# Performance work log

Hardware: AMD Instinct MI355X
Metric: run time of the kernel (lower is better)

## Reference

```python
import jax, jax.numpy as jnp
import numpy as np

H = 16      # num_heads
D = 64      # internal_emb_dim (head dim)
E = 1024    # q/kv input embedding dim
NEG_INF = float('-inf')


def setup_inputs() -> dict:
    key = jax.random.key(0)
    ks = jax.random.split(key, 10)
    B, S = 2, 2048
    sc_in = 1.0 / np.sqrt(E)            # kaiming-uniform-ish scale
    sc_h = 1.0 / np.sqrt(H * D)
    return {
        'x':    jax.random.normal(ks[0], (B, S, E), jnp.float32),
        'ln_g': jnp.ones((E,), jnp.float32),
        'ln_b': jnp.zeros((E,), jnp.float32),
        # weights stored [in, out] (transpose of torch layout), biases zero-init per module
        'wq': jax.random.uniform(ks[1], (E, H * D), jnp.float32, -sc_in, sc_in),
        'bq': jnp.zeros((H * D,), jnp.float32),
        'wk': jax.random.uniform(ks[2], (E, H * D), jnp.float32, -sc_in, sc_in),
        'bk': jnp.zeros((H * D,), jnp.float32),
        'wv': jax.random.uniform(ks[3], (E, H * D), jnp.float32, -sc_in, sc_in),
        'bv': jnp.zeros((H * D,), jnp.float32),
        'w0': jax.random.uniform(ks[4], (H * D, E), jnp.float32, -sc_h, sc_h),
        'b0': jnp.zeros((E,), jnp.float32),
    }


def _layer_norm(x, g, b, eps=1e-5):
    mu = jnp.mean(x, axis=-1, keepdims=True)
    var = jnp.mean(jnp.square(x - mu), axis=-1, keepdims=True)
    return (x - mu) * jax.lax.rsqrt(var + eps) * g + b


def reference(x, ln_g, ln_b, wq, bq, wk, bk, wv, bv, w0, b0):
    B, S, _ = x.shape
    residual = x
    xn = _layer_norm(x, ln_g, ln_b)
    # projections -> [B, H, S, D]
    q = (xn @ wq + bq).reshape(B, S, H, D).transpose(0, 2, 1, 3)
    k = (xn @ wk + bk).reshape(B, S, H, D).transpose(0, 2, 1, 3)
    v = (xn @ wv + bv).reshape(B, S, H, D).transpose(0, 2, 1, 3)
    scores = jnp.einsum('bhqd,bhkd->bhqk', q, k) / jnp.sqrt(jnp.float32(D))
    # custom mask: strictly lower triangle (j < i) filled with -inf
    mask = jnp.tril(jnp.ones((S, S), bool), k=-1)
    scores = jnp.where(mask, NEG_INF, scores)
    a = jax.nn.softmax(scores, axis=-1)
    h = jnp.einsum('bhqk,bhkd->bhqd', a, v)
    h = h.transpose(0, 2, 1, 3).reshape(B, S, H * D)
    return h @ w0 + b0 + residual
```

## Files before the change

kernel.cpp:

```cpp
#include <hip/hip_runtime.h>
#include <hip/hip_bf16.h>
#include <stdint.h>

#define S_LEN 2048
#define E_DIM 1024
#define NHEAD 16
#define DHEAD 64
#define NB 2
#define NROWS (NB * S_LEN)

typedef __attribute__((ext_vector_type(8))) short bf16x8;
typedef __attribute__((ext_vector_type(4))) float f32x4;

__device__ __forceinline__ unsigned short f2b(float f) {
    union { __hip_bfloat16 h; unsigned short u; } cv;
    cv.h = __float2bfloat16(f);
    return cv.u;
}

__device__ __forceinline__ void gload_lds16(const void* g, void* l) {
    __builtin_amdgcn_global_load_lds(
        (const __attribute__((address_space(1))) unsigned int*)g,
        (__attribute__((address_space(3))) unsigned int*)l, 16, 0, 0);
}

__global__ __launch_bounds__(256) void wtrans_kernel(
    const float* __restrict__ wq, const float* __restrict__ wk,
    const float* __restrict__ wv, const float* __restrict__ w0,
    unsigned short* __restrict__ wqT, unsigned short* __restrict__ wkT,
    unsigned short* __restrict__ wvT, unsigned short* __restrict__ w0T) {
    const int z = blockIdx.z;
    const float* W = (z == 0) ? wq : (z == 1) ? wk : (z == 2) ? wv : w0;
    unsigned short* WT = (z == 0) ? wqT : (z == 1) ? wkT : (z == 2) ? wvT : w0T;
    const int k0 = blockIdx.x * 64;
    const int n0 = blockIdx.y * 64;
    __shared__ float tile[64][69];
    const int t = threadIdx.x;
    const int rowq = t >> 4;
    const int cc4 = (t & 15) * 4;
    #pragma unroll
    for (int rr = 0; rr < 4; ++rr) {
        const int r = rr * 16 + rowq;
        const float4 v = *reinterpret_cast<const float4*>(W + (size_t)(k0 + r) * E_DIM + n0 + cc4);
        tile[r][cc4 + 0] = v.x; tile[r][cc4 + 1] = v.y;
        tile[r][cc4 + 2] = v.z; tile[r][cc4 + 3] = v.w;
    }
    __syncthreads();
    #pragma unroll
    for (int rr = 0; rr < 4; ++rr) {
        const int n = rr * 16 + rowq;
        ushort4 o;
        o.x = f2b(tile[cc4 + 0][n]);
        o.y = f2b(tile[cc4 + 1][n]);
        o.z = f2b(tile[cc4 + 2][n]);
        o.w = f2b(tile[cc4 + 3][n]);
        *reinterpret_cast<ushort4*>(WT + (size_t)(n0 + n) * E_DIM + k0 + cc4) = o;
    }
}

__global__ __launch_bounds__(256) void ln_kernel(const float* __restrict__ x,
    const float* __restrict__ g, const float* __restrict__ bt,
    unsigned short* __restrict__ xn) {
    const int row = blockIdx.x;
    const int t = threadIdx.x;
    const float4 v = reinterpret_cast<const float4*>(x + (size_t)row * E_DIM)[t];
    float s  = v.x + v.y + v.z + v.w;
    float ss = v.x * v.x + v.y * v.y + v.z * v.z + v.w * v.w;
    #pragma unroll
    for (int off = 32; off > 0; off >>= 1) {
        s  += __shfl_down(s, off);
        ss += __shfl_down(ss, off);
    }
    __shared__ float red[8];
    if ((t & 63) == 0) { red[t >> 6] = s; red[(t >> 6) + 4] = ss; }
    __syncthreads();
    s  = red[0] + red[1] + red[2] + red[3];
    ss = red[4] + red[5] + red[6] + red[7];
    const float mu  = s * (1.0f / E_DIM);
    const float var = ss * (1.0f / E_DIM) - mu * mu;
    const float rs  = rsqrtf(var + 1e-5f);
    const float4 gv = reinterpret_cast<const float4*>(g)[t];
    const float4 bv = reinterpret_cast<const float4*>(bt)[t];
    ushort4 o;
    o.x = f2b((v.x - mu) * rs * gv.x + bv.x);
    o.y = f2b((v.y - mu) * rs * gv.y + bv.y);
    o.z = f2b((v.z - mu) * rs * gv.z + bv.z);
    o.w = f2b((v.w - mu) * rs * gv.w + bv.w);
    reinterpret_cast<ushort4*>(xn + (size_t)row * E_DIM)[t] = o;
}

__device__ __forceinline__ void gemm128_mainloop(
    const unsigned short* __restrict__ A, const unsigned short* __restrict__ BT,
    int m0, int n0, unsigned short* As, unsigned short* Bs, f32x4 acc[4][4]) {
    const int t = threadIdx.x;
    const int l = t & 63;
    const int w = t >> 6;
    const int wr = w >> 1, wc = w & 1;
    const int lr = l >> 3;
    const int gs = (l & 7) ^ lr;
    const int il = l & 15;
    const int kq = l >> 4;

    for (int kt = 0; kt < E_DIM; kt += 64) {
        __syncthreads();
        #pragma unroll
        for (int c = 0; c < 4; ++c) {
            const int cc = w * 4 + c;
            gload_lds16(A + (size_t)(m0 + cc * 8 + lr) * E_DIM + kt + gs * 8, As + cc * 512);
        }
        #pragma unroll
        for (int c = 0; c < 4; ++c) {
            const int cc = w * 4 + c;
            gload_lds16(BT + (size_t)(n0 + cc * 8 + lr) * E_DIM + kt + gs * 8, Bs + cc * 512);
        }
        __syncthreads();
        #pragma unroll
        for (int ks = 0; ks < 2; ++ks) {
            bf16x8 af[4], bfr[4];
            #pragma unroll
            for (int mi = 0; mi < 4; ++mi) {
                const int r = wr * 64 + mi * 16 + il;
                af[mi] = *reinterpret_cast<const bf16x8*>(As + r * 64 + ((ks * 4 + kq) ^ (r & 7)) * 8);
            }
            #pragma unroll
            for (int ni = 0; ni < 4; ++ni) {
                const int r = wc * 64 + ni * 16 + il;
                bfr[ni] = *reinterpret_cast<const bf16x8*>(Bs + r * 64 + ((ks * 4 + kq) ^ (r & 7)) * 8);
            }
            #pragma unroll
            for (int mi = 0; mi < 4; ++mi)
                #pragma unroll
                for (int ni = 0; ni < 4; ++ni)
                    acc[mi][ni] = __builtin_amdgcn_mfma_f32_16x16x32_bf16(af[mi], bfr[ni], acc[mi][ni], 0, 0, 0);
        }
    }
}

__global__ __launch_bounds__(256) void qkv_kernel(
    const unsigned short* __restrict__ xn,
    const unsigned short* __restrict__ wqT, const float* __restrict__ bq,
    const unsigned short* __restrict__ wkT, const float* __restrict__ bk,
    const unsigned short* __restrict__ wvT, const float* __restrict__ bv,
    unsigned short* __restrict__ qo, unsigned short* __restrict__ ko,
    unsigned short* __restrict__ vo) {
    __shared__ __align__(16) unsigned short As[8192];
    __shared__ __align__(16) unsigned short Bs[8192];
    const int mat = blockIdx.z;
    const unsigned short* BT = (mat == 0) ? wqT : (mat == 1) ? wkT : wvT;
    const float* bias = (mat == 0) ? bq : (mat == 1) ? bk : bv;
    const int m0 = blockIdx.x * 128, n0 = blockIdx.y * 128;

    const f32x4 ZERO = {0.f, 0.f, 0.f, 0.f};
    f32x4 acc[4][4];
    #pragma unroll
    for (int i = 0; i < 4; ++i)
        #pragma unroll
        for (int j = 0; j < 4; ++j) acc[i][j] = ZERO;

    gemm128_mainloop(xn, BT, m0, n0, As, Bs, acc);

    const int t = threadIdx.x, l = t & 63, w = t >> 6;
    const int wr = w >> 1, wc = w & 1;
    const int il = l & 15, kq = l >> 4;
    const int b = m0 >> 11;
    const float qsc = (mat == 0) ? 0.125f : 1.0f;
    unsigned short* outp = (mat == 0) ? qo : ko;

    #pragma unroll
    for (int ni = 0; ni < 4; ++ni) {
        const int n = n0 + wc * 64 + ni * 16 + il;
        const int h = n >> 6, d = n & 63;
        const float bb = bias[n];
        #pragma unroll
        for (int mi = 0; mi < 4; ++mi) {
            const int mbase = m0 + wr * 64 + mi * 16 + kq * 4;
            const int sbase = mbase & (S_LEN - 1);
            if (mat == 2) {
                ushort4 o;
                o.x = f2b(acc[mi][ni][0] + bb);
                o.y = f2b(acc[mi][ni][1] + bb);
                o.z = f2b(acc[mi][ni][2] + bb);
                o.w = f2b(acc[mi][ni][3] + bb);
                *reinterpret_cast<ushort4*>(vo + ((size_t)(b * NHEAD + h) * DHEAD + d) * S_LEN + sbase) = o;
            } else {
                #pragma unroll
                for (int r = 0; r < 4; ++r)
                    outp[((size_t)(b * NHEAD + h) * S_LEN + sbase + r) * DHEAD + d] =
                        f2b((acc[mi][ni][r] + bb) * qsc);
            }
        }
    }
}

__device__ __forceinline__ void attn_tile128(
    const unsigned short* __restrict__ Kc, const unsigned short* __restrict__ Vc,
    unsigned short* __restrict__ Pw, const bf16x8* qf,
    float* m, float* lsum, f32x4* o,
    int il, int kq, int w, int qi0, int kt0, bool do_mask) {
    const f32x4 ZERO = {0.f, 0.f, 0.f, 0.f};
    f32x4 s[8];
    #pragma unroll
    for (int nf = 0; nf < 8; ++nf) s[nf] = ZERO;
    #pragma unroll
    for (int ks = 0; ks < 2; ++ks)
        #pragma unroll
        for (int nf = 0; nf < 8; ++nf) {
            const int j = nf * 16 + il;
            const bf16x8 kf = *reinterpret_cast<const bf16x8*>(
                Kc + j * 64 + (((ks * 4 + kq) ^ (il & 7)) * 8));
            s[nf] = __builtin_amdgcn_mfma_f32_16x16x32_bf16(qf[ks], kf, s[nf], 0, 0, 0);
        }
    if (do_mask) {
        #pragma unroll
        for (int nf = 0; nf < 8; ++nf) {
            const int j = kt0 + nf * 16 + il;
            #pragma unroll
            for (int r = 0; r < 4; ++r) {
                const int i = qi0 + w * 16 + kq * 4 + r;
                if (j < i) s[nf][r] = -INFINITY;
            }
        }
    }
    float tm[4];
    #pragma unroll
    for (int r = 0; r < 4; ++r) {
        float v = s[0][r];
        #pragma unroll
        for (int nf = 1; nf < 8; ++nf) v = fmaxf(v, s[nf][r]);
        tm[r] = v;
    }
    #pragma unroll
    for (int msk = 8; msk; msk >>= 1)
        #pragma unroll
        for (int r = 0; r < 4; ++r)
            tm[r] = fmaxf(tm[r], __shfl_xor(tm[r], msk));
    float sc_[4];
    #pragma unroll
    for (int r = 0; r < 4; ++r) {
        const float nm = fmaxf(m[r], tm[r]);
        sc_[r] = __expf(m[r] - nm);
        m[r] = nm;
    }
    float ps[4] = {0.f, 0.f, 0.f, 0.f};
    #pragma unroll
    for (int nf = 0; nf < 8; ++nf)
        #pragma unroll
        for (int r = 0; r < 4; ++r) {
            const float pv = __expf(s[nf][r] - m[r]);
            ps[r] += pv;
            const int i = kq * 4 + r;
            const int col = nf * 16 + il;
            Pw[i * 128 + (((col >> 3) ^ i) * 8) + (col & 7)] = f2b(pv);
        }
    #pragma unroll
    for (int msk = 8; msk; msk >>= 1)
        #pragma unroll
        for (int r = 0; r < 4; ++r)
            ps[r] += __shfl_xor(ps[r], msk);
    #pragma unroll
    for (int r = 0; r < 4; ++r) lsum[r] = lsum[r] * sc_[r] + ps[r];
    #pragma unroll
    for (int nf = 0; nf < 4; ++nf)
        #pragma unroll
        for (int r = 0; r < 4; ++r) o[nf][r] *= sc_[r];
    asm volatile("s_waitcnt lgkmcnt(0)" ::: "memory");
    #pragma unroll
    for (int ks = 0; ks < 4; ++ks) {
        const bf16x8 pa = *reinterpret_cast<const bf16x8*>(
            Pw + il * 128 + (((ks * 4 + kq) ^ il) * 8));
        #pragma unroll
        for (int nf = 0; nf < 4; ++nf) {
            const int dl = nf * 16 + il;
            const bf16x8 vf = *reinterpret_cast<const bf16x8*>(
                Vc + dl * 128 + (((ks * 4 + kq) ^ il) * 8));
            o[nf] = __builtin_amdgcn_mfma_f32_16x16x32_bf16(pa, vf, o[nf], 0, 0, 0);
        }
    }
}

__global__ __launch_bounds__(256) void attn_kernel(
    const unsigned short* __restrict__ q,
    const unsigned short* __restrict__ k,
    const unsigned short* __restrict__ vt,
    unsigned short* __restrict__ hb) {
    __shared__ __align__(16) unsigned short Ks[2][8192];
    __shared__ __align__(16) unsigned short Vs[2][8192];
    __shared__ __align__(16) unsigned short Ps[8192];
    const int qtA = blockIdx.x;
    const int bh  = blockIdx.y;
    const int qiA = qtA * 64;
    const int qiB = (31 - qtA) * 64;
    const int startA = qiA & ~127;
    const int startB = qiB & ~127;
    const unsigned short* qp = q + (size_t)bh * S_LEN * DHEAD;
    const unsigned short* kp = k + (size_t)bh * S_LEN * DHEAD;
    const unsigned short* vp = vt + (size_t)bh * DHEAD * S_LEN;
    const int t = threadIdx.x, l = t & 63, w = t >> 6;
    const int il = l & 15, kq = l >> 4;
    const int lr = l >> 3, kls = l & 7;
    const int vr = l >> 4, vs = l & 15;

    auto stage = [&](int buf, int kt) {
        #pragma unroll
        for (int c = 0; c < 4; ++c) {
            const int cc = w * 4 + c;
            const int krow = cc * 8 + lr;
            gload_lds16(kp + (size_t)(kt + krow) * DHEAD + (kls ^ lr) * 8, &Ks[buf][cc * 512]);
            const int vrow = cc * 4 + vr;
            gload_lds16(vp + (size_t)vrow * S_LEN + kt + (vs ^ (vrow & 15)) * 8, &Vs[buf][cc * 512]);
        }
    };

    const f32x4 ZERO = {0.f, 0.f, 0.f, 0.f};
    bf16x8 qfA[2], qfB[2];
    {
        const int rA = qiA + w * 16 + il;
        const int rB = qiB + w * 16 + il;
        qfA[0] = *reinterpret_cast<const bf16x8*>(qp + (size_t)rA * DHEAD + kq * 8);
        qfA[1] = *reinterpret_cast<const bf16x8*>(qp + (size_t)rA * DHEAD + 32 + kq * 8);
        qfB[0] = *reinterpret_cast<const bf16x8*>(qp + (size_t)rB * DHEAD + kq * 8);
        qfB[1] = *reinterpret_cast<const bf16x8*>(qp + (size_t)rB * DHEAD + 32 + kq * 8);
    }

    float mA[4], lA[4], mB[4], lB[4];
    f32x4 oA[4], oB[4];
    #pragma unroll
    for (int r = 0; r < 4; ++r) { mA[r] = -INFINITY; lA[r] = 0.f; mB[r] = -INFINITY; lB[r] = 0.f; }
    #pragma unroll
    for (int nf = 0; nf < 4; ++nf) { oA[nf] = ZERO; oB[nf] = ZERO; }

    unsigned short* Pw = Ps + w * 2048;

    stage(0, startA);
    __syncthreads();
    int cur = 0;

    for (int kt0 = startA; kt0 < S_LEN; kt0 += 128) {
        if (kt0 + 128 < S_LEN) stage(cur ^ 1, kt0 + 128);
        attn_tile128(Ks[cur], Vs[cur], Pw, qfA, mA, lA, oA, il, kq, w, qiA, kt0, kt0 == startA);
        if (kt0 >= startB)
            attn_tile128(Ks[cur], Vs[cur], Pw, qfB, mB, lB, oB, il, kq, w, qiB, kt0, kt0 == startB);
        __syncthreads();
        cur ^= 1;
    }

    const int b = bh >> 4, hh = bh & 15;
    float rlA[4], rlB[4];
    #pragma unroll
    for (int r = 0; r < 4; ++r) { rlA[r] = 1.0f / lA[r]; rlB[r] = 1.0f / lB[r]; }
    #pragma unroll
    for (int nf = 0; nf < 4; ++nf) {
        const int col = hh * 64 + nf * 16 + il;
        #pragma unroll
        for (int r = 0; r < 4; ++r) {
            const int rowA = qiA + w * 16 + kq * 4 + r;
            const int rowB = qiB + w * 16 + kq * 4 + r;
            hb[(size_t)(b * S_LEN + rowA) * E_DIM + col] = f2b(oA[nf][r] * rlA[r]);
            hb[(size_t)(b * S_LEN + rowB) * E_DIM + col] = f2b(oB[nf][r] * rlB[r]);
        }
    }
}

__global__ __launch_bounds__(256) void oproj_kernel(
    const unsigned short* __restrict__ hbuf, const unsigned short* __restrict__ w0T,
    const float* __restrict__ b0, const float* __restrict__ x,
    float* __restrict__ out) {
    __shared__ __align__(16) unsigned short As[8192];
    __shared__ __align__(16) unsigned short Bs[8192];
    const int m0 = blockIdx.x * 128, n0 = blockIdx.y * 128;

    const f32x4 ZERO = {0.f, 0.f, 0.f, 0.f};
    f32x4 acc[4][4];
    #pragma unroll
    for (int i = 0; i < 4; ++i)
        #pragma unroll
        for (int j = 0; j < 4; ++j) acc[i][j] = ZERO;

    gemm128_mainloop(hbuf, w0T, m0, n0, As, Bs, acc);

    const int t = threadIdx.x, l = t & 63, w = t >> 6;
    const int wr = w >> 1, wc = w & 1;
    const int il = l & 15, kq = l >> 4;
    #pragma unroll
    for (int ni = 0; ni < 4; ++ni) {
        const int n = n0 + wc * 64 + ni * 16 + il;
        const float bb = b0[n];
        #pragma unroll
        for (int mi = 0; mi < 4; ++mi) {
            const int mbase = m0 + wr * 64 + mi * 16 + kq * 4;
            #pragma unroll
            for (int r = 0; r < 4; ++r) {
                const size_t idx = (size_t)(mbase + r) * E_DIM + n;
                out[idx] = acc[mi][ni][r] + bb + x[idx];
            }
        }
    }
}

extern "C" void kernel_launch(void* const* d_in, const int* in_sizes, int n_in,
                              void* d_out, int out_size, void* d_ws, size_t ws_size,
                              hipStream_t stream) {
    (void)in_sizes; (void)n_in; (void)out_size; (void)ws_size;
    const float* x    = (const float*)d_in[0];
    const float* ln_g = (const float*)d_in[1];
    const float* ln_b = (const float*)d_in[2];
    const float* wq   = (const float*)d_in[3];
    const float* bq   = (const float*)d_in[4];
    const float* wk   = (const float*)d_in[5];
    const float* bk   = (const float*)d_in[6];
    const float* wv   = (const float*)d_in[7];
    const float* bv   = (const float*)d_in[8];
    const float* w0   = (const float*)d_in[9];
    const float* b0   = (const float*)d_in[10];

    uint8_t* ws = (uint8_t*)d_ws;
    unsigned short* xnb = (unsigned short*)(ws);
    unsigned short* qb  = (unsigned short*)(ws + (8u  << 20));
    unsigned short* kb  = (unsigned short*)(ws + (16u << 20));
    unsigned short* vtb = (unsigned short*)(ws + (24u << 20));
    unsigned short* wqT = (unsigned short*)(ws + (32u << 20));
    unsigned short* wkT = (unsigned short*)(ws + (34u << 20));
    unsigned short* wvT = (unsigned short*)(ws + (36u << 20));
    unsigned short* w0T = (unsigned short*)(ws + (38u << 20));
    unsigned short* hbf = xnb;

    hipLaunchKernelGGL(wtrans_kernel, dim3(16, 16, 4), dim3(256), 0, stream,
                       wq, wk, wv, w0, wqT, wkT, wvT, w0T);
    hipLaunchKernelGGL(ln_kernel, dim3(NROWS), dim3(256), 0, stream, x, ln_g, ln_b, xnb);
    hipLaunchKernelGGL(qkv_kernel, dim3(32, 8, 3), dim3(256), 0, stream,
                       xnb, wqT, bq, wkT, bk, wvT, bv, qb, kb, vtb);
    hipLaunchKernelGGL(attn_kernel, dim3(16, 32), dim3(256), 0, stream, qb, kb, vtb, hbf);
    hipLaunchKernelGGL(oproj_kernel, dim3(32, 8), dim3(256), 0, stream,
                       hbf, w0T, b0, x, (float*)d_out);
}
```

Baseline: 248.1 us.

## Transpose QK^T MFMA layout, add lazy softmax rescaling and MFMA priority hints

```diff
diff --git a/kernel.cpp b/kernel.cpp
--- a/kernel.cpp
+++ b/kernel.cpp
@@ -195,12 +195,13 @@
 __device__ __forceinline__ void attn_tile128(
     const unsigned short* __restrict__ Kc, const unsigned short* __restrict__ Vc,
     unsigned short* __restrict__ Pw, const bf16x8* qf,
-    float* m, float* lsum, f32x4* o,
+    float& m, float& lsum, f32x4* o,
     int il, int kq, int w, int qi0, int kt0, bool do_mask) {
     const f32x4 ZERO = {0.f, 0.f, 0.f, 0.f};
     f32x4 s[8];
     #pragma unroll
     for (int nf = 0; nf < 8; ++nf) s[nf] = ZERO;
+    __builtin_amdgcn_s_setprio(1);
     #pragma unroll
     for (int ks = 0; ks < 2; ++ks)
         #pragma unroll
@@ -208,74 +209,77 @@
             const int j = nf * 16 + il;
             const bf16x8 kf = *reinterpret_cast<const bf16x8*>(
                 Kc + j * 64 + (((ks * 4 + kq) ^ (il & 7)) * 8));
-            s[nf] = __builtin_amdgcn_mfma_f32_16x16x32_bf16(qf[ks], kf, s[nf], 0, 0, 0);
-        }
+            s[nf] = __builtin_amdgcn_mfma_f32_16x16x32_bf16(kf, qf[ks], s[nf], 0, 0, 0);
+        }
+    __builtin_amdgcn_s_setprio(0);
     if (do_mask) {
-        #pragma unroll
-        for (int nf = 0; nf < 8; ++nf) {
-            const int j = kt0 + nf * 16 + il;
+        const int i = qi0 + w * 16 + il;
+        #pragma unroll
+        for (int nf = 0; nf < 8; ++nf)
             #pragma unroll
             for (int r = 0; r < 4; ++r) {
-                const int i = qi0 + w * 16 + kq * 4 + r;
+                const int j = kt0 + nf * 16 + kq * 4 + r;
                 if (j < i) s[nf][r] = -INFINITY;
             }
-        }
-    }
-    float tm[4];
-    #pragma unroll
-    for (int r = 0; r < 4; ++r) {
-        float v = s[0][r];
-        #pragma unroll
-        for (int nf = 1; nf < 8; ++nf) v = fmaxf(v, s[nf][r]);
-        tm[r] = v;
-    }
-    #pragma unroll
-    for (int msk = 8; msk; msk >>= 1)
-        #pragma unroll
-        for (int r = 0; r < 4; ++r)
-            tm[r] = fmaxf(tm[r], __shfl_xor(tm[r], msk));
-    float sc_[4];
-    #pragma unroll
-    for (int r = 0; r < 4; ++r) {
-        const float nm = fmaxf(m[r], tm[r]);
-        sc_[r] = __expf(m[r] - nm);
-        m[r] = nm;
-    }
-    float ps[4] = {0.f, 0.f, 0.f, 0.f};
+    }
+    float tnf[8];
     #pragma unroll
     for (int nf = 0; nf < 8; ++nf)
+        tnf[nf] = fmaxf(fmaxf(s[nf][0], s[nf][1]), fmaxf(s[nf][2], s[nf][3]));
+    float tm = fmaxf(fmaxf(fmaxf(tnf[0], tnf[1]), fmaxf(tnf[2], tnf[3])),
+                     fmaxf(fmaxf(tnf[4], tnf[5]), fmaxf(tnf[6], tnf[7])));
+    tm = fmaxf(tm, __shfl_xor(tm, 16));
+    tm = fmaxf(tm, __shfl_xor(tm, 32));
+
+    float sc = 1.0f;
+    const bool resc = __any(tm > m + 8.0f);
+    if (resc) {
+        const float nm = fmaxf(m, tm);
+        sc = __expf(m - nm);
+        m = nm;
+    }
+
+    float ps0 = 0.f, ps1 = 0.f;
+    #pragma unroll
+    for (int nf = 0; nf < 8; ++nf) {
+        const float e0 = __expf(s[nf][0] - m);
+        const float e1 = __expf(s[nf][1] - m);
+        const float e2 = __expf(s[nf][2] - m);
+        const float e3 = __expf(s[nf][3] - m);
+        ps0 += e0 + e1; ps1 += e2 + e3;
+        ushort4 pk;
+        pk.x = f2b(e0); pk.y = f2b(e1); pk.z = f2b(e2); pk.w = f2b(e3);
+        *reinterpret_cast<ushort4*>(
+            Pw + il * 128 + (((2 * nf + (kq >> 1)) ^ il) << 3) + ((kq & 1) << 2)) = pk;
+    }
+    float ps = ps0 + ps1;
+    ps += __shfl_xor(ps, 16);
+    ps += __shfl_xor(ps, 32);
+    lsum = lsum * sc + ps;
+
+    if (resc) {
         #pragma unroll
         for (int r = 0; r < 4; ++r) {
-            const float pv = __expf(s[nf][r] - m[r]);
-            ps[r] += pv;
-            const int i = kq * 4 + r;
-            const int col = nf * 16 + il;
-            Pw[i * 128 + (((col >> 3) ^ i) * 8) + (col & 7)] = f2b(pv);
-        }
-    #pragma unroll
-    for (int msk = 8; msk; msk >>= 1)
-        #pragma unroll
-        for (int r = 0; r < 4; ++r)
-            ps[r] += __shfl_xor(ps[r], msk);
-    #pragma unroll
-    for (int r = 0; r < 4; ++r) lsum[r] = lsum[r] * sc_[r] + ps[r];
-    #pragma unroll
-    for (int nf = 0; nf < 4; ++nf)
-        #pragma unroll
-        for (int r = 0; r < 4; ++r) o[nf][r] *= sc_[r];
-    asm volatile("s_waitcnt lgkmcnt(0)" ::: "memory");
+            const float scq = __shfl(sc, kq * 4 + r);
+            #pragma unroll
+            for (int nf = 0; nf < 4; ++nf) o[nf][r] *= scq;
+        }
+    }
+
+    __builtin_amdgcn_s_setprio(1);
     #pragma unroll
     for (int ks = 0; ks < 4; ++ks) {
         const bf16x8 pa = *reinterpret_cast<const bf16x8*>(
-            Pw + il * 128 + (((ks * 4 + kq) ^ il) * 8));
+            Pw + il * 128 + (((ks * 4 + kq) ^ il) << 3));
         #pragma unroll
         for (int nf = 0; nf < 4; ++nf) {
             const int dl = nf * 16 + il;
             const bf16x8 vf = *reinterpret_cast<const bf16x8*>(
-                Vc + dl * 128 + (((ks * 4 + kq) ^ il) * 8));
+                Vc + dl * 128 + (((ks * 4 + kq) ^ il) << 3));
             o[nf] = __builtin_amdgcn_mfma_f32_16x16x32_bf16(pa, vf, o[nf], 0, 0, 0);
         }
     }
+    __builtin_amdgcn_s_setprio(0);
 }
 
 __global__ __launch_bounds__(256) void attn_kernel(
@@ -322,10 +326,8 @@
         qfB[1] = *reinterpret_cast<const bf16x8*>(qp + (size_t)rB * DHEAD + 32 + kq * 8);
     }
 
-    float mA[4], lA[4], mB[4], lB[4];
+    float mA = -INFINITY, lA = 0.f, mB = -INFINITY, lB = 0.f;
     f32x4 oA[4], oB[4];
-    #pragma unroll
-    for (int r = 0; r < 4; ++r) { mA[r] = -INFINITY; lA[r] = 0.f; mB[r] = -INFINITY; lB[r] = 0.f; }
     #pragma unroll
     for (int nf = 0; nf < 4; ++nf) { oA[nf] = ZERO; oB[nf] = ZERO; }
 
@@ -345,9 +347,13 @@
     }
 
     const int b = bh >> 4, hh = bh & 15;
+    const float rvA = 1.0f / lA, rvB = 1.0f / lB;
     float rlA[4], rlB[4];
     #pragma unroll
-    for (int r = 0; r < 4; ++r) { rlA[r] = 1.0f / lA[r]; rlB[r] = 1.0f / lB[r]; }
+    for (int r = 0; r < 4; ++r) {
+        rlA[r] = __shfl(rvA, kq * 4 + r);
+        rlB[r] = __shfl(rvB, kq * 4 + r);
+    }
     #pragma unroll
     for (int nf = 0; nf < 4; ++nf) {
         const int col = hh * 64 + nf * 16 + il;
```

Result: faster. 214.0 us (-13.7%).
